# Kernel optimization log

Hardware: AMD Instinct MI355X
Metric: run time of the kernel (lower is better)

Reference implementation:

```python
import jax, jax.numpy as jnp
import numpy as np

NUM_NODES = 8192
IN_FEATURES = 1024
OUT_FEATURES = 512
NUM_EDGES = 262144  # avg degree 32


def setup_inputs() -> dict:
    key = jax.random.key(0)
    k_x, k_w, k_b, k_src, k_dst = jax.random.split(key, 5)
    x = jax.random.normal(k_x, (NUM_NODES, IN_FEATURES), dtype=jnp.float32)
    # torch nn.Linear layout: weight [out, in], bias [out]
    W = jax.random.normal(k_w, (OUT_FEATURES, IN_FEATURES), dtype=jnp.float32) * (1.0 / np.sqrt(IN_FEATURES))
    b = jax.random.normal(k_b, (OUT_FEATURES,), dtype=jnp.float32) * 0.01
    src = jax.random.randint(k_src, (NUM_EDGES,), 0, NUM_NODES, dtype=jnp.int64)
    dst = jax.random.randint(k_dst, (NUM_EDGES,), 0, NUM_NODES, dtype=jnp.int64)
    edge_index = jnp.stack([src, dst], axis=0)
    return {"x": x, "W": W, "b": b, "edge_index": edge_index, "num_nodes": NUM_NODES}


def reference(x, W, b, edge_index, num_nodes):
    # Faithful to the torch module: build dense adjacency from edge list
    # (duplicate edges collapse to 1.0 via assignment semantics),
    # linear, (dropout p=0 -> identity), dense adj @ hidden, relu.
    adj = jnp.zeros((num_nodes, num_nodes), dtype=x.dtype)
    adj = adj.at[edge_index[0], edge_index[1]].set(1.0)
    hidden = x @ W.T + b            # [N, out]
    support = adj @ hidden          # [N, out] aggregation over neighbors
    return jax.nn.relu(support)
```

## Files before the change

kernel.cpp:

```cpp
#include <hip/hip_runtime.h>

#define N_NODES 8192
#define IN_F    1024
#define OUT_F   512
#define N_EDGES 262144
#define STRIDE  96

#define HID_OFF     0u
#define XB_OFF      8388608u
#define WB_OFF      25165824u
#define DEG_OFF     26214400u
#define COL_OFF     26247168u
#define MAX_DEG     STRIDE

typedef short  bf16x8 __attribute__((ext_vector_type(8)));
typedef float  f32x4  __attribute__((ext_vector_type(4)));

__device__ __forceinline__ unsigned short f2bf(float f) {
    unsigned u = __float_as_uint(f);
    u += 0x7fffu + ((u >> 16) & 1u);
    return (unsigned short)(u >> 16);
}

__device__ __forceinline__ float bflo(unsigned u) { return __uint_as_float(u << 16); }
__device__ __forceinline__ float bfhi(unsigned u) { return __uint_as_float(u & 0xffff0000u); }

__device__ __forceinline__ void ld_lds16(const void* g, void* l) {
    __builtin_amdgcn_global_load_lds(
        (const __attribute__((address_space(1))) void*)g,
        (__attribute__((address_space(3))) void*)l, 16, 0, 0);
}

#define NX8 (N_NODES * IN_F / 8)
#define NW8 (OUT_F * IN_F / 8)
__global__ __launch_bounds__(256) void cvt_bf16_all(const float* __restrict__ x,
                                                    const float* __restrict__ w,
                                                    unsigned short* __restrict__ xb,
                                                    int* __restrict__ deg) {
    int i = blockIdx.x * blockDim.x + threadIdx.x;
    if (i < N_NODES) deg[i] = 0;
    if (i >= NX8 + NW8) return;
    const f32x4* p = (i < NX8) ? ((const f32x4*)x + (size_t)i * 2)
                               : ((const f32x4*)w + (size_t)(i - NX8) * 2);
    f32x4 v0 = __builtin_nontemporal_load(p);
    f32x4 v1 = __builtin_nontemporal_load(p + 1);
    uint4 o;
    o.x = (unsigned)f2bf(v0.x) | ((unsigned)f2bf(v0.y) << 16);
    o.y = (unsigned)f2bf(v0.z) | ((unsigned)f2bf(v0.w) << 16);
    o.z = (unsigned)f2bf(v1.x) | ((unsigned)f2bf(v1.y) << 16);
    o.w = (unsigned)f2bf(v1.z) | ((unsigned)f2bf(v1.w) << 16);
    *((uint4*)xb + i) = o;
}

#define GEMM_BLOCKS 512

__global__ __launch_bounds__(256, 2) void gemm_scatter(const unsigned short* __restrict__ Xb,
                                                       const unsigned short* __restrict__ Wb,
                                                       const float* __restrict__ bias,
                                                       unsigned short* __restrict__ H,
                                                       const int* __restrict__ src,
                                                       const int* __restrict__ dst,
                                                       int* __restrict__ deg,
                                                       int* __restrict__ col) {
    __shared__ unsigned short As[2][128 * 64];
    __shared__ unsigned short Bs[2][64 * 64];

    const int bid = blockIdx.x;
    const int tid = threadIdx.x;

    if (bid >= GEMM_BLOCKS) {
        int e = (bid - GEMM_BLOCKS) * 256 + tid;
        int s = src[e];
        int slot = atomicAdd(&deg[s], 1);
        if (slot < STRIDE) col[s * STRIDE + slot] = dst[e];
        return;
    }

    const int lane = tid & 63;
    const int wave = tid >> 6;
    const int row0 = (bid & 63) * 128;
    const int col0 = (bid >> 6) * 64;
    const int wm   = (wave & 1) * 64;
    const int wn   = (wave >> 1) * 32;
    const int fm   = lane & 15;
    const int fm7  = fm & 7;
    const int q    = lane >> 4;

    f32x4 acc[4][2];
#pragma unroll
    for (int i = 0; i < 4; ++i)
#pragma unroll
        for (int j = 0; j < 2; ++j) acc[i][j] = (f32x4)0.f;

    const int r0 = tid >> 3;
    const int kp = ((tid & 7) ^ (r0 & 7)) * 8;
    const unsigned short* Xbase = Xb + (size_t)(row0 + r0) * IN_F + kp;
    const unsigned short* Wbase = Wb + (size_t)(col0 + r0) * IN_F + kp;

#define STAGE(buf, k0) do {                                                   \
    ld_lds16(Xbase            + (k0), &As[buf][tid * 8]);                     \
    ld_lds16(Xbase + 32*IN_F  + (k0), &As[buf][(tid + 256) * 8]);             \
    ld_lds16(Xbase + 64*IN_F  + (k0), &As[buf][(tid + 512) * 8]);             \
    ld_lds16(Xbase + 96*IN_F  + (k0), &As[buf][(tid + 768) * 8]);             \
    ld_lds16(Wbase            + (k0), &Bs[buf][tid * 8]);                     \
    ld_lds16(Wbase + 32*IN_F  + (k0), &Bs[buf][(tid + 256) * 8]);             \
} while (0)

#define COMPUTE(buf) do {                                                     \
    _Pragma("unroll")                                                         \
    for (int s = 0; s < 2; ++s) {                                             \
        const int kq = s * 4 + q;                                             \
        bf16x8 a[4], b[2];                                                    \
        _Pragma("unroll")                                                     \
        for (int mi = 0; mi < 4; ++mi)                                        \
            a[mi] = *(const bf16x8*)&As[buf][(((wm + mi*16 + fm) << 3) + (kq ^ fm7)) << 3]; \
        _Pragma("unroll")                                                     \
        for (int ni = 0; ni < 2; ++ni)                                        \
            b[ni] = *(const bf16x8*)&Bs[buf][(((wn + ni*16 + fm) << 3) + (kq ^ fm7)) << 3]; \
        _Pragma("unroll")                                                     \
        for (int mi = 0; mi < 4; ++mi)                                        \
            _Pragma("unroll")                                                 \
            for (int ni = 0; ni < 2; ++ni)                                    \
                acc[mi][ni] = __builtin_amdgcn_mfma_f32_16x16x32_bf16(        \
                    a[mi], b[ni], acc[mi][ni], 0, 0, 0);                      \
    }                                                                         \
} while (0)

    STAGE(0, 0);
    __syncthreads();
    int cur = 0;
    for (int t = 0; t < 15; ++t) {
        STAGE(cur ^ 1, (t + 1) * 64);
        COMPUTE(cur);
        __syncthreads();
        cur ^= 1;
    }
    COMPUTE(cur);

    const int cm = (lane >> 4) * 4;
#pragma unroll
    for (int ni = 0; ni < 2; ++ni) {
        const int c = col0 + wn + ni * 16 + fm;
        const float bv = bias[c];
#pragma unroll
        for (int mi = 0; mi < 4; ++mi) {
#pragma unroll
            for (int r = 0; r < 4; ++r) {
                const int row = row0 + wm + mi * 16 + cm + r;
                H[(size_t)row * OUT_F + c] = f2bf(acc[mi][ni][r] + bv);
            }
        }
    }
#undef STAGE
#undef COMPUTE
}

__global__ __launch_bounds__(256, 8) void aggregate(const unsigned short* __restrict__ H,
                                                    const int* __restrict__ dg,
                                                    const int* __restrict__ col,
                                                    float* __restrict__ out) {
    __shared__ int nbr[4][MAX_DEG];
    __shared__ int uniq[4][MAX_DEG];
    __shared__ int wcnt[4];
    const int wave = threadIdx.x >> 6;
    const int lane = threadIdx.x & 63;
    const int task = blockIdx.x * 4 + wave;
    const int v    = task >> 1;
    const int half = task & 1;
    int d = dg[v];
    if (d > MAX_DEG) d = MAX_DEG;

    if (lane == 0) wcnt[wave] = 0;
    int id0 = -1, id1 = -1;
    if (lane < d)      { id0 = col[v * STRIDE + lane];      nbr[wave][lane]      = id0; }
    if (64 + lane < d) { id1 = col[v * STRIDE + 64 + lane]; nbr[wave][64 + lane] = id1; }
    __builtin_amdgcn_wave_barrier();

    bool k0 = (lane < d);
    const int lim0 = k0 ? lane : 0;
    for (int j = 0; j < lim0; ++j) k0 = k0 & (nbr[wave][j] != id0);
    bool k1 = (64 + lane < d);
    const int lim1 = k1 ? (64 + lane) : 0;
    for (int j = 0; j < lim1; ++j) k1 = k1 & (nbr[wave][j] != id1);
    if (k0) uniq[wave][atomicAdd(&wcnt[wave], 1)] = id0;
    if (k1) uniq[wave][atomicAdd(&wcnt[wave], 1)] = id1;
    __builtin_amdgcn_wave_barrier();
    const int n  = wcnt[wave];
    const int* uq = &uniq[wave][0];
    const unsigned short* Hh = H + half * 256 + lane * 4;

    float a0=0,a1=0,a2=0,a3=0;
    int e = 0;
    for (; e + 12 <= n; e += 12) {
        uint2 h[12];
#pragma unroll
        for (int t = 0; t < 12; ++t)
            h[t] = *(const uint2*)&Hh[(size_t)uq[e + t] * OUT_F];
#pragma unroll
        for (int t = 0; t < 12; ++t) {
            a0 += bflo(h[t].x); a1 += bfhi(h[t].x);
            a2 += bflo(h[t].y); a3 += bfhi(h[t].y);
        }
    }
    for (; e + 4 <= n; e += 4) {
        uint2 h[4];
#pragma unroll
        for (int t = 0; t < 4; ++t)
            h[t] = *(const uint2*)&Hh[(size_t)uq[e + t] * OUT_F];
#pragma unroll
        for (int t = 0; t < 4; ++t) {
            a0 += bflo(h[t].x); a1 += bfhi(h[t].x);
            a2 += bflo(h[t].y); a3 += bfhi(h[t].y);
        }
    }
    for (; e < n; ++e) {
        uint2 h0 = *(const uint2*)&Hh[(size_t)uq[e] * OUT_F];
        a0 += bflo(h0.x); a1 += bfhi(h0.x);
        a2 += bflo(h0.y); a3 += bfhi(h0.y);
    }
    f32x4 o = {fmaxf(a0,0.f), fmaxf(a1,0.f), fmaxf(a2,0.f), fmaxf(a3,0.f)};
    __builtin_nontemporal_store(o, (f32x4*)&out[(size_t)v * OUT_F + half * 256 + lane * 4]);
}

extern "C" void kernel_launch(void* const* d_in, const int* in_sizes, int n_in,
                              void* d_out, int out_size, void* d_ws, size_t ws_size,
                              hipStream_t stream) {
    const float* x  = (const float*)d_in[0];
    const float* W  = (const float*)d_in[1];
    const float* b  = (const float*)d_in[2];
    const int*   ei = (const int*)d_in[3];
    float* out = (float*)d_out;

    char* ws = (char*)d_ws;
    unsigned short* H   = (unsigned short*)(ws + HID_OFF);
    unsigned short* Xb  = (unsigned short*)(ws + XB_OFF);
    unsigned short* Wb  = (unsigned short*)(ws + WB_OFF);
    int*            deg = (int*)(ws + DEG_OFF);
    int*            col = (int*)(ws + COL_OFF);

    cvt_bf16_all<<<(NX8 + NW8 + 255) / 256, 256, 0, stream>>>(x, W, Xb, deg);

    gemm_scatter<<<GEMM_BLOCKS + N_EDGES / 256, 256, 0, stream>>>(
        Xb, Wb, b, H, ei, ei + N_EDGES, deg, col);

    aggregate<<<N_NODES * 2 / 4, 256, 0, stream>>>(H, deg, col, out);
}
```

Baseline: 139.6 us.

## Split neighbor dedup into separate kernel and quarter output columns in aggregate

Moves the per-node duplicate-neighbor removal out of the aggregation kernel into a dedicated dedup kernel that writes unique neighbor lists and counts to workspace. Before, each node's dedup ran twice, once per half-column task; now it runs once per node. The aggregate kernel then splits each node's 512 columns into four 128-column slices, with each lane loading 4 bytes instead of 8. This doubles the block count and deepens the unroll to 16. It costs an extra kernel launch, a workspace round trip for the unique lists, and narrower per-lane loads.

```diff
diff --git a/kernel.cpp b/kernel.cpp
--- a/kernel.cpp
+++ b/kernel.cpp
@@ -11,10 +11,13 @@
 #define WB_OFF      25165824u
 #define DEG_OFF     26214400u
 #define COL_OFF     26247168u
+#define UCNT_OFF    29392896u
+#define UCOL_OFF    29425664u
 #define MAX_DEG     STRIDE
 
 typedef short  bf16x8 __attribute__((ext_vector_type(8)));
 typedef float  f32x4  __attribute__((ext_vector_type(4)));
+typedef float  f32x2  __attribute__((ext_vector_type(2)));
 
 __device__ __forceinline__ unsigned short f2bf(float f) {
     unsigned u = __float_as_uint(f);
@@ -155,18 +158,15 @@
 #undef COMPUTE
 }
 
-__global__ __launch_bounds__(256, 8) void aggregate(const unsigned short* __restrict__ H,
-                                                    const int* __restrict__ dg,
-                                                    const int* __restrict__ col,
-                                                    float* __restrict__ out) {
+__global__ __launch_bounds__(256) void dedup(const int* __restrict__ dg,
+                                             const int* __restrict__ col,
+                                             int* __restrict__ ucol,
+                                             int* __restrict__ ucnt) {
     __shared__ int nbr[4][MAX_DEG];
-    __shared__ int uniq[4][MAX_DEG];
     __shared__ int wcnt[4];
     const int wave = threadIdx.x >> 6;
     const int lane = threadIdx.x & 63;
-    const int task = blockIdx.x * 4 + wave;
-    const int v    = task >> 1;
-    const int half = task & 1;
+    const int v    = blockIdx.x * 4 + wave;
     int d = dg[v];
     if (d > MAX_DEG) d = MAX_DEG;
 
@@ -182,44 +182,49 @@
     bool k1 = (64 + lane < d);
     const int lim1 = k1 ? (64 + lane) : 0;
     for (int j = 0; j < lim1; ++j) k1 = k1 & (nbr[wave][j] != id1);
-    if (k0) uniq[wave][atomicAdd(&wcnt[wave], 1)] = id0;
-    if (k1) uniq[wave][atomicAdd(&wcnt[wave], 1)] = id1;
+    if (k0) ucol[v * STRIDE + atomicAdd(&wcnt[wave], 1)] = id0;
+    if (k1) ucol[v * STRIDE + atomicAdd(&wcnt[wave], 1)] = id1;
     __builtin_amdgcn_wave_barrier();
-    const int n  = wcnt[wave];
-    const int* uq = &uniq[wave][0];
-    const unsigned short* Hh = H + half * 256 + lane * 4;
-
-    float a0=0,a1=0,a2=0,a3=0;
+    if (lane == 0) ucnt[v] = wcnt[wave];
+}
+
+__global__ __launch_bounds__(256, 8) void aggregate(const unsigned short* __restrict__ H,
+                                                    const int* __restrict__ ucnt,
+                                                    const int* __restrict__ ucol,
+                                                    float* __restrict__ out) {
+    const int wave = threadIdx.x >> 6;
+    const int lane = threadIdx.x & 63;
+    const int bid  = blockIdx.x;
+    const int q    = bid & 3;
+    const int v    = (bid >> 2) * 4 + wave;
+    const int n    = ucnt[v];
+    const int* uq  = ucol + v * STRIDE;
+    const unsigned short* Hq = H + q * 128 + lane * 2;
+
+    float a0 = 0.f, a1 = 0.f;
     int e = 0;
-    for (; e + 12 <= n; e += 12) {
-        uint2 h[12];
-#pragma unroll
-        for (int t = 0; t < 12; ++t)
-            h[t] = *(const uint2*)&Hh[(size_t)uq[e + t] * OUT_F];
-#pragma unroll
-        for (int t = 0; t < 12; ++t) {
-            a0 += bflo(h[t].x); a1 += bfhi(h[t].x);
-            a2 += bflo(h[t].y); a3 += bfhi(h[t].y);
-        }
+    for (; e + 16 <= n; e += 16) {
+        unsigned h[16];
+#pragma unroll
+        for (int t = 0; t < 16; ++t)
+            h[t] = *(const unsigned*)&Hq[(size_t)uq[e + t] * OUT_F];
+#pragma unroll
+        for (int t = 0; t < 16; ++t) { a0 += bflo(h[t]); a1 += bfhi(h[t]); }
     }
     for (; e + 4 <= n; e += 4) {
-        uint2 h[4];
+        unsigned h[4];
 #pragma unroll
         for (int t = 0; t < 4; ++t)
-            h[t] = *(const uint2*)&Hh[(size_t)uq[e + t] * OUT_F];
-#pragma unroll
-        for (int t = 0; t < 4; ++t) {
-            a0 += bflo(h[t].x); a1 += bfhi(h[t].x);
-            a2 += bflo(h[t].y); a3 += bfhi(h[t].y);
-        }
+            h[t] = *(const unsigned*)&Hq[(size_t)uq[e + t] * OUT_F];
+#pragma unroll
+        for (int t = 0; t < 4; ++t) { a0 += bflo(h[t]); a1 += bfhi(h[t]); }
     }
     for (; e < n; ++e) {
-        uint2 h0 = *(const uint2*)&Hh[(size_t)uq[e] * OUT_F];
-        a0 += bflo(h0.x); a1 += bfhi(h0.x);
-        a2 += bflo(h0.y); a3 += bfhi(h0.y);
-    }
-    f32x4 o = {fmaxf(a0,0.f), fmaxf(a1,0.f), fmaxf(a2,0.f), fmaxf(a3,0.f)};
-    __builtin_nontemporal_store(o, (f32x4*)&out[(size_t)v * OUT_F + half * 256 + lane * 4]);
+        unsigned h = *(const unsigned*)&Hq[(size_t)uq[e] * OUT_F];
+        a0 += bflo(h); a1 += bfhi(h);
+    }
+    f32x2 o = {fmaxf(a0, 0.f), fmaxf(a1, 0.f)};
+    __builtin_nontemporal_store(o, (f32x2*)&out[(size_t)v * OUT_F + q * 128 + lane * 2]);
 }
 
 extern "C" void kernel_launch(void* const* d_in, const int* in_sizes, int n_in,
@@ -232,16 +237,20 @@
     float* out = (float*)d_out;
 
     char* ws = (char*)d_ws;
-    unsigned short* H   = (unsigned short*)(ws + HID_OFF);
-    unsigned short* Xb  = (unsigned short*)(ws + XB_OFF);
-    unsigned short* Wb  = (unsigned short*)(ws + WB_OFF);
-    int*            deg = (int*)(ws + DEG_OFF);
-    int*            col = (int*)(ws + COL_OFF);
+    unsigned short* H    = (unsigned short*)(ws + HID_OFF);
+    unsigned short* Xb   = (unsigned short*)(ws + XB_OFF);
+    unsigned short* Wb   = (unsigned short*)(ws + WB_OFF);
+    int*            deg  = (int*)(ws + DEG_OFF);
+    int*            col  = (int*)(ws + COL_OFF);
+    int*            ucnt = (int*)(ws + UCNT_OFF);
+    int*            ucol = (int*)(ws + UCOL_OFF);
 
     cvt_bf16_all<<<(NX8 + NW8 + 255) / 256, 256, 0, stream>>>(x, W, Xb, deg);
 
     gemm_scatter<<<GEMM_BLOCKS + N_EDGES / 256, 256, 0, stream>>>(
         Xb, Wb, b, H, ei, ei + N_EDGES, deg, col);
 
-    aggregate<<<N_NODES * 2 / 4, 256, 0, stream>>>(H, deg, col, out);
-}
+    dedup<<<N_NODES / 4, 256, 0, stream>>>(deg, col, ucol, ucnt);
+
+    aggregate<<<N_NODES * 4 / 4, 256, 0, stream>>>(H, ucnt, ucol, out);
+}
```

Measured after the change: 140.6 us. No clear change (+0.7%).
